# Optimization experiments

Measured on AMD Instinct MI355X. Metric: run time of the kernel, lower is better.

## Reference

```python
import jax, jax.numpy as jnp
import numpy as np

B, T, D = 4, 2048, 2048
P, K, ALPHA, R = 512, 16, 4, 32
E_RATIO = 0.8
EPS = 1e-6


def rmsnorm(x, g):
    return x * jax.lax.rsqrt(jnp.mean(x * x, axis=-1, keepdims=True) + EPS) * g


def dale_signs():
    # first e_ratio*P neurons excitatory (+1), rest inhibitory (-1)
    return jnp.where(jnp.arange(P) < int(E_RATIO * P), 1.0, -1.0)


def quant_dale(w, signs):
    # STE sign-quantization with per-neuron mean-abs scale + Dale's-law sign constraint
    scale = jnp.mean(jnp.abs(w), axis=-1, keepdims=True)  # [P,1]
    q = scale * signs[:, None] * jnp.ones_like(w)         # magnitude=scale, sign fixed per neuron
    return w + jax.lax.stop_gradient(q - w)


def synapse_graph(x, idx, w):
    # x: [B,T,D], idx: [P,K] int, w: [P,K] -> dendritic inputs [B,T,P,K]
    return jnp.take(x, idx, axis=-1) * w


def perceptron(x_dend, Wp, Wout, signs):
    Wq = quant_dale(Wp, signs)                              # [P,K]
    u = jnp.einsum('btpk,pk->btp', x_dend, Wq)              # [B,T,P]
    f = jax.nn.sigmoid(u)                                   # gate [B,T,P]
    f_out = quant_dale(Wout, signs)                         # [P,ALPHA]
    y = (f * u)[..., None] * f_out                          # [B,T,P,ALPHA]
    return u, f, y, f_out


def low_rank_ssm(t, f, s0, U, V, Wgate, bgate):
    # t,f: [B,T,P]; s0: [B,R]. Low-rank gated linear scan in R dims.
    z = jnp.einsum('btp,pr->btr', t, U)
    lam = jax.nn.sigmoid(jnp.einsum('btp,pr->btr', f, Wgate) + bgate)

    def step(s, inp):
        z_t, l_t = inp
        s = l_t * s + z_t
        return s, s

    sT, S = jax.lax.scan(step, s0, (jnp.moveaxis(z, 1, 0), jnp.moveaxis(lam, 1, 0)))
    tilde = jnp.einsum('btr,rp->btp', jnp.moveaxis(S, 0, 1), V)
    return tilde, sT


def flatten_ports(y):
    return y.reshape(*y.shape[:-2], P * ALPHA)


def setup_inputs() -> dict:
    key = jax.random.key(0)
    ks = jax.random.split(key, 14)
    sc = 0.1
    return {
        'x': jax.random.normal(ks[0], (B, T, D), jnp.float32),
        'state': jnp.zeros((B, R), jnp.float32),
        'g1': jnp.ones((D,), jnp.float32),
        'g2': jnp.ones((D,), jnp.float32),
        'idx_ssm': jax.random.randint(ks[1], (P, K), 0, D),
        'wg_ssm': jax.random.normal(ks[2], (P, K), jnp.float32) * sc,
        'idx_mlp': jax.random.randint(ks[3], (P, K), 0, D),
        'wg_mlp': jax.random.normal(ks[4], (P, K), jnp.float32) * sc,
        'Wp_ssm': jax.random.normal(ks[5], (P, K), jnp.float32) * sc,
        'Wout_ssm': jax.random.normal(ks[6], (P, ALPHA), jnp.float32) * sc,
        'Wp_mlp': jax.random.normal(ks[7], (P, K), jnp.float32) * sc,
        'Wout_mlp': jax.random.normal(ks[8], (P, ALPHA), jnp.float32) * sc,
        'U': jax.random.normal(ks[9], (P, R), jnp.float32) * sc,
        'V': jax.random.normal(ks[10], (R, P), jnp.float32) * sc,
        'Wgate': jax.random.normal(ks[11], (P, R), jnp.float32) * sc,
        'bgate': jnp.zeros((R,), jnp.float32),
    }


def reference(x, state, g1, g2, idx_ssm, wg_ssm, idx_mlp, wg_mlp,
              Wp_ssm, Wout_ssm, Wp_mlp, Wout_mlp, U, V, Wgate, bgate):
    signs = dale_signs()
    # --- SSM branch ---
    h1 = rmsnorm(x, g1)
    x_dend_ssm = synapse_graph(h1, idx_ssm, wg_ssm)
    u_ssm, f_ssm, _, f_out = perceptron(x_dend_ssm, Wp_ssm, Wout_ssm, signs)
    t_ssm = f_ssm * u_ssm
    tilde_t, new_state = low_rank_ssm(t_ssm, f_ssm, state, U, V, Wgate, bgate)
    y_ssm = (f_ssm * tilde_t)[..., None] * f_out            # [B,T,P,ALPHA]
    x_after = x + flatten_ports(y_ssm)
    # --- MLP branch ---
    h2 = rmsnorm(x_after, g2)
    x_dend_mlp = synapse_graph(h2, idx_mlp, wg_mlp)
    _, _, y_mlp, _ = perceptron(x_dend_mlp, Wp_mlp, Wout_mlp, signs)
    x_out = x_after + flatten_ports(y_mlp)
    return x_out, new_state
```

## Files before the change

### kernel.cpp

```cpp
#include <hip/hip_runtime.h>
#include <hip/hip_bf16.h>

#define B_ 4
#define T_ 2048
#define D_ 2048
#define P_ 512
#define K_ 16
#define ALPHA_ 4
#define R_ 32
#define NE_ 409
#define EPS_ 1e-6f
#define G_ 4

typedef unsigned short u16;
typedef unsigned int u32;
typedef _Float16 half2_t __attribute__((ext_vector_type(2)));

__device__ __forceinline__ float sigmoidf_(float x) {
  return 1.0f / (1.0f + __expf(-x));
}
__device__ __forceinline__ float bfb2f(u16 u) {
  return __uint_as_float(((u32)u) << 16);
}
__device__ __forceinline__ u16 f2bfb(float f) {
  __hip_bfloat16 h = __float2bfloat16(f);
  return *reinterpret_cast<u16*>(&h);
}
__device__ __forceinline__ float bflo(u32 u) { return __uint_as_float(u << 16); }
__device__ __forceinline__ float bfhi(u32 u) { return __uint_as_float(u & 0xFFFF0000u); }
__device__ __forceinline__ u16 f2h(float f) {
  _Float16 h = (_Float16)f;
  return *reinterpret_cast<u16*>(&h);
}
__device__ __forceinline__ float dot2h(u32 a, u32 b, float c) {
#if __has_builtin(__builtin_amdgcn_fdot2)
  return __builtin_amdgcn_fdot2(__builtin_bit_cast(half2_t, a),
                                __builtin_bit_cast(half2_t, b), c, false);
#else
  half2_t ha = __builtin_bit_cast(half2_t, a);
  half2_t hb = __builtin_bit_cast(half2_t, b);
  return c + (float)ha.x * (float)hb.x + (float)ha.y * (float)hb.y;
#endif
}

__global__ void k_scalars(const float* __restrict__ Wp_s, const float* __restrict__ Wo_s,
                          const float* __restrict__ Wp_m, const float* __restrict__ Wo_m,
                          const float* __restrict__ U, const float* __restrict__ Wgt,
                          float* __restrict__ wq_s, float* __restrict__ fo_s,
                          float* __restrict__ wq_m, float* __restrict__ fo_m,
                          u16* __restrict__ Ut16, u16* __restrict__ Wt16) {
  int p = blockIdx.x * blockDim.x + threadIdx.x;
  if (p >= P_) return;
  float sgn = (p < NE_) ? 1.0f : -1.0f;
  float a = 0, b = 0, c = 0, d = 0;
#pragma unroll
  for (int k = 0; k < K_; k++) {
    a += fabsf(Wp_s[p * K_ + k]);
    c += fabsf(Wp_m[p * K_ + k]);
  }
#pragma unroll
  for (int k = 0; k < ALPHA_; k++) {
    b += fabsf(Wo_s[p * ALPHA_ + k]);
    d += fabsf(Wo_m[p * ALPHA_ + k]);
  }
  wq_s[p] = sgn * a * (1.0f / K_);
  fo_s[p] = sgn * b * (1.0f / ALPHA_);
  wq_m[p] = sgn * c * (1.0f / K_);
  fo_m[p] = sgn * d * (1.0f / ALPHA_);
#pragma unroll
  for (int r = 0; r < R_; r++) {
    Ut16[r * P_ + p] = f2h(U[p * R_ + r]);
    Wt16[r * P_ + p] = f2h(Wgt[p * R_ + r]);
  }
}

__global__ __launch_bounds__(256) void k_phase1(
    const float* __restrict__ x, const float* __restrict__ g1,
    const int* __restrict__ idx, const float* __restrict__ wg,
    const u16* __restrict__ Ut16, const u16* __restrict__ Wt16,
    const float* __restrict__ bg, const float* __restrict__ wq,
    u16* __restrict__ f_ssm, float* __restrict__ z, float* __restrict__ lam) {
  __shared__ u16 h1[G_][D_];
  __shared__ u16 tl16[G_][P_];
  __shared__ u16 fl16[G_][P_];
  __shared__ float red[G_][4];
  __shared__ float zp[G_][R_][4];
  __shared__ float lp[G_][R_][4];

  int tid = threadIdx.x;
  int token0 = blockIdx.x * G_;
  int b = token0 >> 11;
  int t0 = token0 & (T_ - 1);

  float gv[8];
  {
    const float4* gp = reinterpret_cast<const float4*>(g1 + tid * 8);
    *reinterpret_cast<float4*>(&gv[0]) = gp[0];
    *reinterpret_cast<float4*>(&gv[4]) = gp[1];
  }
#pragma unroll
  for (int tok = 0; tok < G_; tok++) {
    float xv[8];
    const float4* xp = reinterpret_cast<const float4*>(x + (size_t)(token0 + tok) * D_ + tid * 8);
    *reinterpret_cast<float4*>(&xv[0]) = xp[0];
    *reinterpret_cast<float4*>(&xv[4]) = xp[1];
    float ss = 0;
    u16 tmp[8];
#pragma unroll
    for (int i = 0; i < 8; i++) { ss += xv[i] * xv[i]; tmp[i] = f2bfb(xv[i] * gv[i]); }
    *reinterpret_cast<uint4*>(&h1[tok][tid * 8]) = *reinterpret_cast<const uint4*>(tmp);
#pragma unroll
    for (int off = 32; off; off >>= 1) ss += __shfl_down(ss, off);
    if ((tid & 63) == 0) red[tok][tid >> 6] = ss;
  }
  __syncthreads();

  float inv[G_];
#pragma unroll
  for (int tok = 0; tok < G_; tok++)
    inv[tok] = rsqrtf((red[tok][0] + red[tok][1] + red[tok][2] + red[tok][3]) * (1.0f / D_) + EPS_);

#pragma unroll
  for (int j = 0; j < 2; j++) {
    int p = tid + j * 256;
    union { int4 v[4]; int s[16]; } iu;
    const int4* ip = reinterpret_cast<const int4*>(idx + p * K_);
    iu.v[0] = ip[0]; iu.v[1] = ip[1]; iu.v[2] = ip[2]; iu.v[3] = ip[3];
    union { float4 v[4]; float s[16]; } wu;
    const float4* wp = reinterpret_cast<const float4*>(wg + p * K_);
    wu.v[0] = wp[0]; wu.v[1] = wp[1]; wu.v[2] = wp[2]; wu.v[3] = wp[3];
    float wqp = wq[p];
#pragma unroll
    for (int tok = 0; tok < G_; tok++) {
      float acc = 0;
#pragma unroll
      for (int k = 0; k < K_; k++) acc += bfb2f(h1[tok][iu.s[k]]) * wu.s[k];
      float u = wqp * inv[tok] * acc;
      float f = sigmoidf_(u);
      tl16[tok][p] = f2h(f * u);
      fl16[tok][p] = f2h(f);
      f_ssm[(size_t)(token0 + tok) * P_ + p] = f2bfb(f);
    }
  }
  __syncthreads();

  int r = tid & 31, g = tid >> 5;
  float zs[G_], ls[G_];
#pragma unroll
  for (int tok = 0; tok < G_; tok++) { zs[tok] = 0; ls[tok] = 0; }
  int pb = g * 64;
  const uint4* Utp = reinterpret_cast<const uint4*>(Ut16 + r * P_ + pb);
  const uint4* Wtp = reinterpret_cast<const uint4*>(Wt16 + r * P_ + pb);
#pragma unroll
  for (int q = 0; q < 8; q++) {
    uint4 uq = Utp[q];
    uint4 wq4 = Wtp[q];
#pragma unroll
    for (int tok = 0; tok < G_; tok++) {
      uint4 tq = *reinterpret_cast<const uint4*>(&tl16[tok][pb + q * 8]);
      uint4 fq = *reinterpret_cast<const uint4*>(&fl16[tok][pb + q * 8]);
      zs[tok] = dot2h(tq.x, uq.x, zs[tok]);
      zs[tok] = dot2h(tq.y, uq.y, zs[tok]);
      zs[tok] = dot2h(tq.z, uq.z, zs[tok]);
      zs[tok] = dot2h(tq.w, uq.w, zs[tok]);
      ls[tok] = dot2h(fq.x, wq4.x, ls[tok]);
      ls[tok] = dot2h(fq.y, wq4.y, ls[tok]);
      ls[tok] = dot2h(fq.z, wq4.z, ls[tok]);
      ls[tok] = dot2h(fq.w, wq4.w, ls[tok]);
    }
  }
#pragma unroll
  for (int tok = 0; tok < G_; tok++) {
    zs[tok] += __shfl_down(zs[tok], 32);
    ls[tok] += __shfl_down(ls[tok], 32);
  }
  int wid = tid >> 6;
  if ((tid & 63) < 32) {
#pragma unroll
    for (int tok = 0; tok < G_; tok++) { zp[tok][r][wid] = zs[tok]; lp[tok][r][wid] = ls[tok]; }
  }
  __syncthreads();
  if (tid < R_) {
    float bgr = bg[tid];
    float z4[G_], l4[G_];
#pragma unroll
    for (int tok = 0; tok < G_; tok++) {
      float zz = zp[tok][tid][0] + zp[tok][tid][1] + zp[tok][tid][2] + zp[tok][tid][3];
      float ll = lp[tok][tid][0] + lp[tok][tid][1] + lp[tok][tid][2] + lp[tok][tid][3];
      z4[tok] = zz;
      l4[tok] = sigmoidf_(ll + bgr);
    }
    size_t o = ((size_t)(b * R_ + tid)) * T_ + t0;
    *reinterpret_cast<float4*>(&z[o]) = *reinterpret_cast<const float4*>(z4);
    *reinterpret_cast<float4*>(&lam[o]) = *reinterpret_cast<const float4*>(l4);
  }
}

__global__ __launch_bounds__(64) void k_scan(
    const float* __restrict__ z, const float* __restrict__ lam,
    const float* __restrict__ state, float* __restrict__ S,
    float* __restrict__ out_state) {
  int br = blockIdx.x;
  int lane = threadIdx.x;
  const float* zr = z + (size_t)br * T_ + lane * 32;
  const float* lr = lam + (size_t)br * T_ + lane * 32;
  float zb[32], lb[32];
#pragma unroll
  for (int i = 0; i < 32; i += 4) {
    *reinterpret_cast<float4*>(&zb[i]) = *reinterpret_cast<const float4*>(&zr[i]);
    *reinterpret_cast<float4*>(&lb[i]) = *reinterpret_cast<const float4*>(&lr[i]);
  }
  float A = 1.0f, Z = 0.0f;
#pragma unroll
  for (int i = 0; i < 32; i++) { Z = lb[i] * Z + zb[i]; A *= lb[i]; }
  for (int off = 1; off < 64; off <<= 1) {
    float Ap = __shfl_up(A, off);
    float Zp = __shfl_up(Z, off);
    if (lane >= off) { Z = A * Zp + Z; A = A * Ap; }
  }
  float s0 = state[br];
  float Ae = __shfl_up(A, 1);
  float Ze = __shfl_up(Z, 1);
  float s = (lane == 0) ? s0 : (Ae * s0 + Ze);
  float sb[32];
#pragma unroll
  for (int i = 0; i < 32; i++) { s = lb[i] * s + zb[i]; sb[i] = s; }
  float* Sr = S + (size_t)br * T_ + lane * 32;
#pragma unroll
  for (int i = 0; i < 32; i += 4)
    *reinterpret_cast<float4*>(&Sr[i]) = *reinterpret_cast<const float4*>(&sb[i]);
  if (lane == 63) out_state[br] = s;
}

__global__ __launch_bounds__(256) void k_phase3(
    const float* __restrict__ x, const float* __restrict__ g2,
    const int* __restrict__ idx, const float* __restrict__ wg,
    const float* __restrict__ V, const float* __restrict__ S,
    const u16* __restrict__ f_ssm, const float* __restrict__ fo_s,
    const float* __restrict__ wq_m, const float* __restrict__ fo_m,
    float* __restrict__ out) {
  __shared__ float Sl[G_][R_];
  __shared__ u16 h2[G_][D_];
  __shared__ float red[G_][4];

  int tid = threadIdx.x;
  int token0 = blockIdx.x * G_;
  int b = token0 >> 11;
  int t0 = token0 & (T_ - 1);
  int p0 = 2 * tid;

  if (tid < G_ * R_) {
    int tok = tid >> 5, r = tid & 31;
    Sl[tok][r] = S[((size_t)(b * R_ + r)) * T_ + t0 + tok];
  }
  __syncthreads();

  float til0[G_], til1[G_];
#pragma unroll
  for (int tok = 0; tok < G_; tok++) { til0[tok] = 0; til1[tok] = 0; }
#pragma unroll 4
  for (int r = 0; r < R_; r++) {
    float2 vv = *reinterpret_cast<const float2*>(V + r * P_ + p0);
#pragma unroll
    for (int tok = 0; tok < G_; tok++) {
      float s = Sl[tok][r];
      til0[tok] += s * vv.x;
      til1[tok] += s * vv.y;
    }
  }

  float2 fo = *reinterpret_cast<const float2*>(fo_s + p0);
  float gv[8];
  {
    const float4* gp = reinterpret_cast<const float4*>(g2 + tid * 8);
    *reinterpret_cast<float4*>(&gv[0]) = gp[0];
    *reinterpret_cast<float4*>(&gv[4]) = gp[1];
  }

  float xa[G_][8];
#pragma unroll
  for (int tok = 0; tok < G_; tok++) {
    u32 ff = *reinterpret_cast<const u32*>(f_ssm + (size_t)(token0 + tok) * P_ + p0);
    float val0 = bflo(ff) * til0[tok] * fo.x;
    float val1 = bfhi(ff) * til1[tok] * fo.y;
    float xv[8];
    const float4* xp = reinterpret_cast<const float4*>(x + (size_t)(token0 + tok) * D_ + tid * 8);
    *reinterpret_cast<float4*>(&xv[0]) = xp[0];
    *reinterpret_cast<float4*>(&xv[4]) = xp[1];
    float ss = 0;
#pragma unroll
    for (int a = 0; a < 4; a++) {
      float v0 = xv[a] + val0;
      float v1 = xv[4 + a] + val1;
      xa[tok][a] = v0;
      xa[tok][4 + a] = v1;
      ss += v0 * v0 + v1 * v1;
    }
    u16 tmp[8];
#pragma unroll
    for (int i = 0; i < 8; i++) tmp[i] = f2bfb(xa[tok][i] * gv[i]);
    *reinterpret_cast<uint4*>(&h2[tok][tid * 8]) = *reinterpret_cast<const uint4*>(tmp);
#pragma unroll
    for (int off = 32; off; off >>= 1) ss += __shfl_down(ss, off);
    if ((tid & 63) == 0) red[tok][tid >> 6] = ss;
  }
  __syncthreads();

  union { int4 v[4]; int s[16]; } iu0, iu1;
  union { float4 v[4]; float s[16]; } wu0, wu1;
  {
    const int4* ip0 = reinterpret_cast<const int4*>(idx + p0 * K_);
    const int4* ip1 = reinterpret_cast<const int4*>(idx + (p0 + 1) * K_);
    const float4* wp0 = reinterpret_cast<const float4*>(wg + p0 * K_);
    const float4* wp1 = reinterpret_cast<const float4*>(wg + (p0 + 1) * K_);
#pragma unroll
    for (int q = 0; q < 4; q++) { iu0.v[q] = ip0[q]; iu1.v[q] = ip1[q]; wu0.v[q] = wp0[q]; wu1.v[q] = wp1[q]; }
  }
  float2 wqm = *reinterpret_cast<const float2*>(wq_m + p0);
  float2 fom = *reinterpret_cast<const float2*>(fo_m + p0);

#pragma unroll
  for (int tok = 0; tok < G_; tok++) {
    float invt = rsqrtf((red[tok][0] + red[tok][1] + red[tok][2] + red[tok][3]) * (1.0f / D_) + EPS_);
    float acc0 = 0, acc1 = 0;
#pragma unroll
    for (int k = 0; k < K_; k++) {
      acc0 += bfb2f(h2[tok][iu0.s[k]]) * wu0.s[k];
      acc1 += bfb2f(h2[tok][iu1.s[k]]) * wu1.s[k];
    }
    float u0 = wqm.x * invt * acc0, u1 = wqm.y * invt * acc1;
    float f0 = sigmoidf_(u0), f1 = sigmoidf_(u1);
    float val0 = f0 * u0 * fom.x, val1 = f1 * u1 * fom.y;
    float ov[8];
#pragma unroll
    for (int a = 0; a < 4; a++) {
      ov[a] = xa[tok][a] + val0;
      ov[4 + a] = xa[tok][4 + a] + val1;
    }
    float4* op = reinterpret_cast<float4*>(out + (size_t)(token0 + tok) * D_ + tid * 8);
    op[0] = *reinterpret_cast<const float4*>(&ov[0]);
    op[1] = *reinterpret_cast<const float4*>(&ov[4]);
  }
}

extern "C" void kernel_launch(void* const* d_in, const int* in_sizes, int n_in,
                              void* d_out, int out_size, void* d_ws, size_t ws_size,
                              hipStream_t stream) {
  const float* x     = (const float*)d_in[0];
  const float* state = (const float*)d_in[1];
  const float* g1    = (const float*)d_in[2];
  const float* g2    = (const float*)d_in[3];
  const int*   idx_s = (const int*)d_in[4];
  const float* wg_s  = (const float*)d_in[5];
  const int*   idx_m = (const int*)d_in[6];
  const float* wg_m  = (const float*)d_in[7];
  const float* Wp_s  = (const float*)d_in[8];
  const float* Wo_s  = (const float*)d_in[9];
  const float* Wp_m  = (const float*)d_in[10];
  const float* Wo_m  = (const float*)d_in[11];
  const float* U     = (const float*)d_in[12];
  const float* V     = (const float*)d_in[13];
  const float* Wgt   = (const float*)d_in[14];
  const float* bg    = (const float*)d_in[15];
  float* out = (float*)d_out;

  char* ws = (char*)d_ws;
  float* wq_s = (float*)(ws + 0);
  float* fo_s = (float*)(ws + 2048);
  float* wq_m = (float*)(ws + 4096);
  float* fo_m = (float*)(ws + 6144);
  u16* Ut16 = (u16*)(ws + 8192);
  u16* Wt16 = (u16*)(ws + 8192 + 32768);
  size_t off = 8192 + 65536;
  u16* f_ssm = (u16*)(ws + off); off += (size_t)B_ * T_ * P_ * 2;
  float* z   = (float*)(ws + off); off += (size_t)B_ * R_ * T_ * 4;
  float* lam = (float*)(ws + off); off += (size_t)B_ * R_ * T_ * 4;
  float* S   = (float*)(ws + off);

  hipLaunchKernelGGL(k_scalars, dim3(2), dim3(256), 0, stream,
                     Wp_s, Wo_s, Wp_m, Wo_m, U, Wgt, wq_s, fo_s, wq_m, fo_m, Ut16, Wt16);
  hipLaunchKernelGGL(k_phase1, dim3(B_ * T_ / G_), dim3(256), 0, stream,
                     x, g1, idx_s, wg_s, Ut16, Wt16, bg, wq_s, f_ssm, z, lam);
  hipLaunchKernelGGL(k_scan, dim3(B_ * R_), dim3(64), 0, stream,
                     z, lam, state, S, out + (size_t)B_ * T_ * D_);
  hipLaunchKernelGGL(k_phase3, dim3(B_ * T_ / G_), dim3(256), 0, stream,
                     x, g2, idx_m, wg_m, V, S, f_ssm, fo_s, wq_m, fo_m, out);
}
```

Before: 221.9 us.

## Fuse all phases into one persistent kernel with grid barriers

Merges the four launches (scalar prep, phase1, scan, phase3) into one persistent kernel of 1024 blocks, each handling two token groups, separated by atomic-counter grid barriers. The SSM gate f is kept in registers across the barrier instead of being written to and re-read from a global f_ssm buffer. This removes launch gaps and the f_ssm round trip. In exchange it depends on all 1024 blocks being co-resident (launch_bounds 256,4) for the spin barrier to be safe, and it adds barrier latency plus an extra memset launch.

```diff
diff --git a/kernel.cpp b/kernel.cpp
--- a/kernel.cpp
+++ b/kernel.cpp
@@ -11,6 +11,8 @@
 #define NE_ 409
 #define EPS_ 1e-6f
 #define G_ 4
+#define GRID_ 1024
+#define NITER_ 2
 
 typedef unsigned short u16;
 typedef unsigned int u32;
@@ -26,12 +28,18 @@
   __hip_bfloat16 h = __float2bfloat16(f);
   return *reinterpret_cast<u16*>(&h);
 }
-__device__ __forceinline__ float bflo(u32 u) { return __uint_as_float(u << 16); }
-__device__ __forceinline__ float bfhi(u32 u) { return __uint_as_float(u & 0xFFFF0000u); }
 __device__ __forceinline__ u16 f2h(float f) {
   _Float16 h = (_Float16)f;
   return *reinterpret_cast<u16*>(&h);
 }
+__device__ __forceinline__ u32 packh(float a, float b) {
+  half2_t h;
+  h.x = (_Float16)a;
+  h.y = (_Float16)b;
+  return __builtin_bit_cast(u32, h);
+}
+__device__ __forceinline__ float hlo(u32 u) { return (float)__builtin_bit_cast(half2_t, u).x; }
+__device__ __forceinline__ float hhi(u32 u) { return (float)__builtin_bit_cast(half2_t, u).y; }
 __device__ __forceinline__ float dot2h(u32 a, u32 b, float c) {
 #if __has_builtin(__builtin_amdgcn_fdot2)
   return __builtin_amdgcn_fdot2(__builtin_bit_cast(half2_t, a),
@@ -43,303 +51,329 @@
 #endif
 }
 
-__global__ void k_scalars(const float* __restrict__ Wp_s, const float* __restrict__ Wo_s,
-                          const float* __restrict__ Wp_m, const float* __restrict__ Wo_m,
-                          const float* __restrict__ U, const float* __restrict__ Wgt,
-                          float* __restrict__ wq_s, float* __restrict__ fo_s,
-                          float* __restrict__ wq_m, float* __restrict__ fo_m,
-                          u16* __restrict__ Ut16, u16* __restrict__ Wt16) {
-  int p = blockIdx.x * blockDim.x + threadIdx.x;
-  if (p >= P_) return;
-  float sgn = (p < NE_) ? 1.0f : -1.0f;
-  float a = 0, b = 0, c = 0, d = 0;
-#pragma unroll
-  for (int k = 0; k < K_; k++) {
-    a += fabsf(Wp_s[p * K_ + k]);
-    c += fabsf(Wp_m[p * K_ + k]);
+__device__ __forceinline__ void grid_barrier(u32* ctr) {
+  __syncthreads();
+  if (threadIdx.x == 0) {
+    __threadfence();
+    atomicAdd(ctr, 1u);
+    int spins = 0;
+    while (__hip_atomic_load(ctr, __ATOMIC_RELAXED, __HIP_MEMORY_SCOPE_AGENT) < (u32)GRID_ &&
+           spins < (1 << 22)) {
+      __builtin_amdgcn_s_sleep(8);
+      ++spins;
+    }
+    __threadfence();
   }
-#pragma unroll
-  for (int k = 0; k < ALPHA_; k++) {
-    b += fabsf(Wo_s[p * ALPHA_ + k]);
-    d += fabsf(Wo_m[p * ALPHA_ + k]);
-  }
-  wq_s[p] = sgn * a * (1.0f / K_);
-  fo_s[p] = sgn * b * (1.0f / ALPHA_);
-  wq_m[p] = sgn * c * (1.0f / K_);
-  fo_m[p] = sgn * d * (1.0f / ALPHA_);
-#pragma unroll
-  for (int r = 0; r < R_; r++) {
-    Ut16[r * P_ + p] = f2h(U[p * R_ + r]);
-    Wt16[r * P_ + p] = f2h(Wgt[p * R_ + r]);
-  }
-}
-
-__global__ __launch_bounds__(256) void k_phase1(
-    const float* __restrict__ x, const float* __restrict__ g1,
-    const int* __restrict__ idx, const float* __restrict__ wg,
-    const u16* __restrict__ Ut16, const u16* __restrict__ Wt16,
-    const float* __restrict__ bg, const float* __restrict__ wq,
-    u16* __restrict__ f_ssm, float* __restrict__ z, float* __restrict__ lam) {
+  __syncthreads();
+}
+
+__global__ __launch_bounds__(256, 4) void k_fused(
+    const float* __restrict__ x, const float* __restrict__ state,
+    const float* __restrict__ g1, const float* __restrict__ g2,
+    const int* __restrict__ idx_s, const float* __restrict__ wg_s,
+    const int* __restrict__ idx_m, const float* __restrict__ wg_m,
+    const float* __restrict__ Wp_s, const float* __restrict__ Wo_s,
+    const float* __restrict__ Wp_m, const float* __restrict__ Wo_m,
+    const float* __restrict__ U, const float* __restrict__ V,
+    const float* __restrict__ Wgt, const float* __restrict__ bg,
+    float* __restrict__ wq_s, float* __restrict__ fo_s,
+    float* __restrict__ wq_m, float* __restrict__ fo_m,
+    u16* __restrict__ Ut16, u16* __restrict__ Wt16,
+    float* __restrict__ z, float* __restrict__ lam, float* __restrict__ S,
+    u32* __restrict__ bar, float* __restrict__ out) {
   __shared__ u16 h1[G_][D_];
   __shared__ u16 tl16[G_][P_];
   __shared__ u16 fl16[G_][P_];
   __shared__ float red[G_][4];
   __shared__ float zp[G_][R_][4];
   __shared__ float lp[G_][R_][4];
+  __shared__ float Sl[G_][R_];
 
   int tid = threadIdx.x;
-  int token0 = blockIdx.x * G_;
-  int b = token0 >> 11;
-  int t0 = token0 & (T_ - 1);
-
-  float gv[8];
+  int bid = blockIdx.x;
+
+  if (bid < 2) {
+    int p = bid * 256 + tid;
+    float sgn = (p < NE_) ? 1.0f : -1.0f;
+    float a = 0, bb = 0, c = 0, d = 0;
+#pragma unroll
+    for (int k = 0; k < K_; k++) {
+      a += fabsf(Wp_s[p * K_ + k]);
+      c += fabsf(Wp_m[p * K_ + k]);
+    }
+#pragma unroll
+    for (int k = 0; k < ALPHA_; k++) {
+      bb += fabsf(Wo_s[p * ALPHA_ + k]);
+      d += fabsf(Wo_m[p * ALPHA_ + k]);
+    }
+    wq_s[p] = sgn * a * (1.0f / K_);
+    fo_s[p] = sgn * bb * (1.0f / ALPHA_);
+    wq_m[p] = sgn * c * (1.0f / K_);
+    fo_m[p] = sgn * d * (1.0f / ALPHA_);
+#pragma unroll
+    for (int r = 0; r < R_; r++) {
+      Ut16[r * P_ + p] = f2h(U[p * R_ + r]);
+      Wt16[r * P_ + p] = f2h(Wgt[p * R_ + r]);
+    }
+  }
+  grid_barrier(bar + 0);
+
+  u32 freg[NITER_][G_];
+#pragma unroll
+  for (int it = 0; it < NITER_; ++it) {
+    int grp = bid + it * GRID_;
+    int token0 = grp * G_;
+    int b = token0 >> 11;
+    int t0 = token0 & (T_ - 1);
+    __syncthreads();
+
+    float gv[8];
+    {
+      const float4* gp = reinterpret_cast<const float4*>(g1 + tid * 8);
+      *reinterpret_cast<float4*>(&gv[0]) = gp[0];
+      *reinterpret_cast<float4*>(&gv[4]) = gp[1];
+    }
+#pragma unroll
+    for (int tok = 0; tok < G_; tok++) {
+      float xv[8];
+      const float4* xp = reinterpret_cast<const float4*>(x + (size_t)(token0 + tok) * D_ + tid * 8);
+      *reinterpret_cast<float4*>(&xv[0]) = xp[0];
+      *reinterpret_cast<float4*>(&xv[4]) = xp[1];
+      float ss = 0;
+      u16 tmp[8];
+#pragma unroll
+      for (int i = 0; i < 8; i++) { ss += xv[i] * xv[i]; tmp[i] = f2bfb(xv[i] * gv[i]); }
+      *reinterpret_cast<uint4*>(&h1[tok][tid * 8]) = *reinterpret_cast<const uint4*>(tmp);
+#pragma unroll
+      for (int off = 32; off; off >>= 1) ss += __shfl_down(ss, off);
+      if ((tid & 63) == 0) red[tok][tid >> 6] = ss;
+    }
+    __syncthreads();
+
+    float inv[G_];
+#pragma unroll
+    for (int tok = 0; tok < G_; tok++)
+      inv[tok] = rsqrtf((red[tok][0] + red[tok][1] + red[tok][2] + red[tok][3]) * (1.0f / D_) + EPS_);
+
+    {
+      int p0 = 2 * tid, p1 = p0 + 1;
+      union { int4 v[4]; int s[16]; } iu0, iu1;
+      union { float4 v[4]; float s[16]; } wu0, wu1;
+      const int4* ip0 = reinterpret_cast<const int4*>(idx_s + p0 * K_);
+      const int4* ip1 = reinterpret_cast<const int4*>(idx_s + p1 * K_);
+      const float4* wp0 = reinterpret_cast<const float4*>(wg_s + p0 * K_);
+      const float4* wp1 = reinterpret_cast<const float4*>(wg_s + p1 * K_);
+#pragma unroll
+      for (int q = 0; q < 4; q++) { iu0.v[q] = ip0[q]; iu1.v[q] = ip1[q]; wu0.v[q] = wp0[q]; wu1.v[q] = wp1[q]; }
+      float2 wq2 = *reinterpret_cast<const float2*>(wq_s + p0);
+#pragma unroll
+      for (int tok = 0; tok < G_; tok++) {
+        float acc0 = 0, acc1 = 0;
+#pragma unroll
+        for (int k = 0; k < K_; k++) {
+          acc0 += bfb2f(h1[tok][iu0.s[k]]) * wu0.s[k];
+          acc1 += bfb2f(h1[tok][iu1.s[k]]) * wu1.s[k];
+        }
+        float u0 = wq2.x * inv[tok] * acc0, u1 = wq2.y * inv[tok] * acc1;
+        float f0 = sigmoidf_(u0), f1 = sigmoidf_(u1);
+        *reinterpret_cast<u32*>(&tl16[tok][p0]) = packh(f0 * u0, f1 * u1);
+        u32 fp = packh(f0, f1);
+        *reinterpret_cast<u32*>(&fl16[tok][p0]) = fp;
+        freg[it][tok] = fp;
+      }
+    }
+    __syncthreads();
+
+    int r = tid & 31, pg = tid >> 5;
+    float zs[G_], ls[G_];
+#pragma unroll
+    for (int tok = 0; tok < G_; tok++) { zs[tok] = 0; ls[tok] = 0; }
+    int pb = pg * 64;
+    const uint4* Utp = reinterpret_cast<const uint4*>(Ut16 + r * P_ + pb);
+    const uint4* Wtp = reinterpret_cast<const uint4*>(Wt16 + r * P_ + pb);
+#pragma unroll
+    for (int q = 0; q < 8; q++) {
+      uint4 uq = Utp[q];
+      uint4 wq4 = Wtp[q];
+#pragma unroll
+      for (int tok = 0; tok < G_; tok++) {
+        uint4 tq = *reinterpret_cast<const uint4*>(&tl16[tok][pb + q * 8]);
+        uint4 fq = *reinterpret_cast<const uint4*>(&fl16[tok][pb + q * 8]);
+        zs[tok] = dot2h(tq.x, uq.x, zs[tok]);
+        zs[tok] = dot2h(tq.y, uq.y, zs[tok]);
+        zs[tok] = dot2h(tq.z, uq.z, zs[tok]);
+        zs[tok] = dot2h(tq.w, uq.w, zs[tok]);
+        ls[tok] = dot2h(fq.x, wq4.x, ls[tok]);
+        ls[tok] = dot2h(fq.y, wq4.y, ls[tok]);
+        ls[tok] = dot2h(fq.z, wq4.z, ls[tok]);
+        ls[tok] = dot2h(fq.w, wq4.w, ls[tok]);
+      }
+    }
+#pragma unroll
+    for (int tok = 0; tok < G_; tok++) {
+      zs[tok] += __shfl_down(zs[tok], 32);
+      ls[tok] += __shfl_down(ls[tok], 32);
+    }
+    int wid = tid >> 6;
+    if ((tid & 63) < 32) {
+#pragma unroll
+      for (int tok = 0; tok < G_; tok++) { zp[tok][r][wid] = zs[tok]; lp[tok][r][wid] = ls[tok]; }
+    }
+    __syncthreads();
+    if (tid < R_) {
+      float bgr = bg[tid];
+      float z4[G_], l4[G_];
+#pragma unroll
+      for (int tok = 0; tok < G_; tok++) {
+        float zz = zp[tok][tid][0] + zp[tok][tid][1] + zp[tok][tid][2] + zp[tok][tid][3];
+        float ll = lp[tok][tid][0] + lp[tok][tid][1] + lp[tok][tid][2] + lp[tok][tid][3];
+        z4[tok] = zz;
+        l4[tok] = sigmoidf_(ll + bgr);
+      }
+      size_t o = ((size_t)(b * R_ + tid)) * T_ + t0;
+      *reinterpret_cast<float4*>(&z[o]) = *reinterpret_cast<const float4*>(z4);
+      *reinterpret_cast<float4*>(&lam[o]) = *reinterpret_cast<const float4*>(l4);
+    }
+  }
+  grid_barrier(bar + 1);
+
   {
-    const float4* gp = reinterpret_cast<const float4*>(g1 + tid * 8);
-    *reinterpret_cast<float4*>(&gv[0]) = gp[0];
-    *reinterpret_cast<float4*>(&gv[4]) = gp[1];
+    int gw = bid * 4 + (tid >> 6);
+    if (bid < 32 && gw < B_ * R_) {
+      int br = gw;
+      int lane = tid & 63;
+      const float* zr = z + (size_t)br * T_ + lane * 32;
+      const float* lr = lam + (size_t)br * T_ + lane * 32;
+      float zb[32], lb[32];
+#pragma unroll
+      for (int i = 0; i < 32; i += 4) {
+        *reinterpret_cast<float4*>(&zb[i]) = *reinterpret_cast<const float4*>(&zr[i]);
+        *reinterpret_cast<float4*>(&lb[i]) = *reinterpret_cast<const float4*>(&lr[i]);
+      }
+      float A = 1.0f, Z = 0.0f;
+#pragma unroll
+      for (int i = 0; i < 32; i++) { Z = lb[i] * Z + zb[i]; A *= lb[i]; }
+      for (int off = 1; off < 64; off <<= 1) {
+        float Ap = __shfl_up(A, off);
+        float Zp = __shfl_up(Z, off);
+        if (lane >= off) { Z = A * Zp + Z; A = A * Ap; }
+      }
+      float s0 = state[br];
+      float Ae = __shfl_up(A, 1);
+      float Ze = __shfl_up(Z, 1);
+      float s = (lane == 0) ? s0 : (Ae * s0 + Ze);
+      float sb[32];
+#pragma unroll
+      for (int i = 0; i < 32; i++) { s = lb[i] * s + zb[i]; sb[i] = s; }
+      float* Sr = S + (size_t)br * T_ + lane * 32;
+#pragma unroll
+      for (int i = 0; i < 32; i += 4)
+        *reinterpret_cast<float4*>(&Sr[i]) = *reinterpret_cast<const float4*>(&sb[i]);
+      if (lane == 63) out[(size_t)B_ * T_ * D_ + br] = s;
+    }
   }
-#pragma unroll
-  for (int tok = 0; tok < G_; tok++) {
-    float xv[8];
-    const float4* xp = reinterpret_cast<const float4*>(x + (size_t)(token0 + tok) * D_ + tid * 8);
-    *reinterpret_cast<float4*>(&xv[0]) = xp[0];
-    *reinterpret_cast<float4*>(&xv[4]) = xp[1];
-    float ss = 0;
-    u16 tmp[8];
-#pragma unroll
-    for (int i = 0; i < 8; i++) { ss += xv[i] * xv[i]; tmp[i] = f2bfb(xv[i] * gv[i]); }
-    *reinterpret_cast<uint4*>(&h1[tok][tid * 8]) = *reinterpret_cast<const uint4*>(tmp);
-#pragma unroll
-    for (int off = 32; off; off >>= 1) ss += __shfl_down(ss, off);
-    if ((tid & 63) == 0) red[tok][tid >> 6] = ss;
-  }
-  __syncthreads();
-
-  float inv[G_];
-#pragma unroll
-  for (int tok = 0; tok < G_; tok++)
-    inv[tok] = rsqrtf((red[tok][0] + red[tok][1] + red[tok][2] + red[tok][3]) * (1.0f / D_) + EPS_);
-
-#pragma unroll
-  for (int j = 0; j < 2; j++) {
-    int p = tid + j * 256;
-    union { int4 v[4]; int s[16]; } iu;
-    const int4* ip = reinterpret_cast<const int4*>(idx + p * K_);
-    iu.v[0] = ip[0]; iu.v[1] = ip[1]; iu.v[2] = ip[2]; iu.v[3] = ip[3];
-    union { float4 v[4]; float s[16]; } wu;
-    const float4* wp = reinterpret_cast<const float4*>(wg + p * K_);
-    wu.v[0] = wp[0]; wu.v[1] = wp[1]; wu.v[2] = wp[2]; wu.v[3] = wp[3];
-    float wqp = wq[p];
+  grid_barrier(bar + 2);
+
+#pragma unroll
+  for (int it = 0; it < NITER_; ++it) {
+    int grp = bid + it * GRID_;
+    int token0 = grp * G_;
+    int b = token0 >> 11;
+    int t0 = token0 & (T_ - 1);
+    int p0 = 2 * tid;
+    __syncthreads();
+    if (tid < G_ * R_) {
+      int tok = tid >> 5, r = tid & 31;
+      Sl[tok][r] = S[((size_t)(b * R_ + r)) * T_ + t0 + tok];
+    }
+    __syncthreads();
+
+    float til0[G_], til1[G_];
+#pragma unroll
+    for (int tok = 0; tok < G_; tok++) { til0[tok] = 0; til1[tok] = 0; }
+#pragma unroll 4
+    for (int r = 0; r < R_; r++) {
+      float2 vv = *reinterpret_cast<const float2*>(V + r * P_ + p0);
+#pragma unroll
+      for (int tok = 0; tok < G_; tok++) {
+        float s = Sl[tok][r];
+        til0[tok] += s * vv.x;
+        til1[tok] += s * vv.y;
+      }
+    }
+
+    float2 fo = *reinterpret_cast<const float2*>(fo_s + p0);
+    float gv[8];
+    {
+      const float4* gp = reinterpret_cast<const float4*>(g2 + tid * 8);
+      *reinterpret_cast<float4*>(&gv[0]) = gp[0];
+      *reinterpret_cast<float4*>(&gv[4]) = gp[1];
+    }
+
+    float xa[G_][8];
 #pragma unroll
     for (int tok = 0; tok < G_; tok++) {
-      float acc = 0;
-#pragma unroll
-      for (int k = 0; k < K_; k++) acc += bfb2f(h1[tok][iu.s[k]]) * wu.s[k];
-      float u = wqp * inv[tok] * acc;
-      float f = sigmoidf_(u);
-      tl16[tok][p] = f2h(f * u);
-      fl16[tok][p] = f2h(f);
-      f_ssm[(size_t)(token0 + tok) * P_ + p] = f2bfb(f);
-    }
-  }
-  __syncthreads();
-
-  int r = tid & 31, g = tid >> 5;
-  float zs[G_], ls[G_];
-#pragma unroll
-  for (int tok = 0; tok < G_; tok++) { zs[tok] = 0; ls[tok] = 0; }
-  int pb = g * 64;
-  const uint4* Utp = reinterpret_cast<const uint4*>(Ut16 + r * P_ + pb);
-  const uint4* Wtp = reinterpret_cast<const uint4*>(Wt16 + r * P_ + pb);
-#pragma unroll
-  for (int q = 0; q < 8; q++) {
-    uint4 uq = Utp[q];
-    uint4 wq4 = Wtp[q];
+      u32 fp = freg[it][tok];
+      float val0 = hlo(fp) * til0[tok] * fo.x;
+      float val1 = hhi(fp) * til1[tok] * fo.y;
+      float xv[8];
+      const float4* xp = reinterpret_cast<const float4*>(x + (size_t)(token0 + tok) * D_ + tid * 8);
+      *reinterpret_cast<float4*>(&xv[0]) = xp[0];
+      *reinterpret_cast<float4*>(&xv[4]) = xp[1];
+      float ss = 0;
+#pragma unroll
+      for (int a = 0; a < 4; a++) {
+        float v0 = xv[a] + val0;
+        float v1 = xv[4 + a] + val1;
+        xa[tok][a] = v0;
+        xa[tok][4 + a] = v1;
+        ss += v0 * v0 + v1 * v1;
+      }
+      u16 tmp[8];
+#pragma unroll
+      for (int i = 0; i < 8; i++) tmp[i] = f2bfb(xa[tok][i] * gv[i]);
+      *reinterpret_cast<uint4*>(&h1[tok][tid * 8]) = *reinterpret_cast<const uint4*>(tmp);
+#pragma unroll
+      for (int off = 32; off; off >>= 1) ss += __shfl_down(ss, off);
+      if ((tid & 63) == 0) red[tok][tid >> 6] = ss;
+    }
+    __syncthreads();
+
+    union { int4 v[4]; int s[16]; } iu0, iu1;
+    union { float4 v[4]; float s[16]; } wu0, wu1;
+    {
+      const int4* ip0 = reinterpret_cast<const int4*>(idx_m + p0 * K_);
+      const int4* ip1 = reinterpret_cast<const int4*>(idx_m + (p0 + 1) * K_);
+      const float4* wp0 = reinterpret_cast<const float4*>(wg_m + p0 * K_);
+      const float4* wp1 = reinterpret_cast<const float4*>(wg_m + (p0 + 1) * K_);
+#pragma unroll
+      for (int q = 0; q < 4; q++) { iu0.v[q] = ip0[q]; iu1.v[q] = ip1[q]; wu0.v[q] = wp0[q]; wu1.v[q] = wp1[q]; }
+    }
+    float2 wqm = *reinterpret_cast<const float2*>(wq_m + p0);
+    float2 fom = *reinterpret_cast<const float2*>(fo_m + p0);
+
 #pragma unroll
     for (int tok = 0; tok < G_; tok++) {
-      uint4 tq = *reinterpret_cast<const uint4*>(&tl16[tok][pb + q * 8]);
-      uint4 fq = *reinterpret_cast<const uint4*>(&fl16[tok][pb + q * 8]);
-      zs[tok] = dot2h(tq.x, uq.x, zs[tok]);
-      zs[tok] = dot2h(tq.y, uq.y, zs[tok]);
-      zs[tok] = dot2h(tq.z, uq.z, zs[tok]);
-      zs[tok] = dot2h(tq.w, uq.w, zs[tok]);
-      ls[tok] = dot2h(fq.x, wq4.x, ls[tok]);
-      ls[tok] = dot2h(fq.y, wq4.y, ls[tok]);
-      ls[tok] = dot2h(fq.z, wq4.z, ls[tok]);
-      ls[tok] = dot2h(fq.w, wq4.w, ls[tok]);
-    }
-  }
-#pragma unroll
-  for (int tok = 0; tok < G_; tok++) {
-    zs[tok] += __shfl_down(zs[tok], 32);
-    ls[tok] += __shfl_down(ls[tok], 32);
-  }
-  int wid = tid >> 6;
-  if ((tid & 63) < 32) {
-#pragma unroll
-    for (int tok = 0; tok < G_; tok++) { zp[tok][r][wid] = zs[tok]; lp[tok][r][wid] = ls[tok]; }
-  }
-  __syncthreads();
-  if (tid < R_) {
-    float bgr = bg[tid];
-    float z4[G_], l4[G_];
-#pragma unroll
-    for (int tok = 0; tok < G_; tok++) {
-      float zz = zp[tok][tid][0] + zp[tok][tid][1] + zp[tok][tid][2] + zp[tok][tid][3];
-      float ll = lp[tok][tid][0] + lp[tok][tid][1] + lp[tok][tid][2] + lp[tok][tid][3];
-      z4[tok] = zz;
-      l4[tok] = sigmoidf_(ll + bgr);
-    }
-    size_t o = ((size_t)(b * R_ + tid)) * T_ + t0;
-    *reinterpret_cast<float4*>(&z[o]) = *reinterpret_cast<const float4*>(z4);
-    *reinterpret_cast<float4*>(&lam[o]) = *reinterpret_cast<const float4*>(l4);
-  }
-}
-
-__global__ __launch_bounds__(64) void k_scan(
-    const float* __restrict__ z, const float* __restrict__ lam,
-    const float* __restrict__ state, float* __restrict__ S,
-    float* __restrict__ out_state) {
-  int br = blockIdx.x;
-  int lane = threadIdx.x;
-  const float* zr = z + (size_t)br * T_ + lane * 32;
-  const float* lr = lam + (size_t)br * T_ + lane * 32;
-  float zb[32], lb[32];
-#pragma unroll
-  for (int i = 0; i < 32; i += 4) {
-    *reinterpret_cast<float4*>(&zb[i]) = *reinterpret_cast<const float4*>(&zr[i]);
-    *reinterpret_cast<float4*>(&lb[i]) = *reinterpret_cast<const float4*>(&lr[i]);
-  }
-  float A = 1.0f, Z = 0.0f;
-#pragma unroll
-  for (int i = 0; i < 32; i++) { Z = lb[i] * Z + zb[i]; A *= lb[i]; }
-  for (int off = 1; off < 64; off <<= 1) {
-    float Ap = __shfl_up(A, off);
-    float Zp = __shfl_up(Z, off);
-    if (lane >= off) { Z = A * Zp + Z; A = A * Ap; }
-  }
-  float s0 = state[br];
-  float Ae = __shfl_up(A, 1);
-  float Ze = __shfl_up(Z, 1);
-  float s = (lane == 0) ? s0 : (Ae * s0 + Ze);
-  float sb[32];
-#pragma unroll
-  for (int i = 0; i < 32; i++) { s = lb[i] * s + zb[i]; sb[i] = s; }
-  float* Sr = S + (size_t)br * T_ + lane * 32;
-#pragma unroll
-  for (int i = 0; i < 32; i += 4)
-    *reinterpret_cast<float4*>(&Sr[i]) = *reinterpret_cast<const float4*>(&sb[i]);
-  if (lane == 63) out_state[br] = s;
-}
-
-__global__ __launch_bounds__(256) void k_phase3(
-    const float* __restrict__ x, const float* __restrict__ g2,
-    const int* __restrict__ idx, const float* __restrict__ wg,
-    const float* __restrict__ V, const float* __restrict__ S,
-    const u16* __restrict__ f_ssm, const float* __restrict__ fo_s,
-    const float* __restrict__ wq_m, const float* __restrict__ fo_m,
-    float* __restrict__ out) {
-  __shared__ float Sl[G_][R_];
-  __shared__ u16 h2[G_][D_];
-  __shared__ float red[G_][4];
-
-  int tid = threadIdx.x;
-  int token0 = blockIdx.x * G_;
-  int b = token0 >> 11;
-  int t0 = token0 & (T_ - 1);
-  int p0 = 2 * tid;
-
-  if (tid < G_ * R_) {
-    int tok = tid >> 5, r = tid & 31;
-    Sl[tok][r] = S[((size_t)(b * R_ + r)) * T_ + t0 + tok];
-  }
-  __syncthreads();
-
-  float til0[G_], til1[G_];
-#pragma unroll
-  for (int tok = 0; tok < G_; tok++) { til0[tok] = 0; til1[tok] = 0; }
-#pragma unroll 4
-  for (int r = 0; r < R_; r++) {
-    float2 vv = *reinterpret_cast<const float2*>(V + r * P_ + p0);
-#pragma unroll
-    for (int tok = 0; tok < G_; tok++) {
-      float s = Sl[tok][r];
-      til0[tok] += s * vv.x;
-      til1[tok] += s * vv.y;
-    }
-  }
-
-  float2 fo = *reinterpret_cast<const float2*>(fo_s + p0);
-  float gv[8];
-  {
-    const float4* gp = reinterpret_cast<const float4*>(g2 + tid * 8);
-    *reinterpret_cast<float4*>(&gv[0]) = gp[0];
-    *reinterpret_cast<float4*>(&gv[4]) = gp[1];
-  }
-
-  float xa[G_][8];
-#pragma unroll
-  for (int tok = 0; tok < G_; tok++) {
-    u32 ff = *reinterpret_cast<const u32*>(f_ssm + (size_t)(token0 + tok) * P_ + p0);
-    float val0 = bflo(ff) * til0[tok] * fo.x;
-    float val1 = bfhi(ff) * til1[tok] * fo.y;
-    float xv[8];
-    const float4* xp = reinterpret_cast<const float4*>(x + (size_t)(token0 + tok) * D_ + tid * 8);
-    *reinterpret_cast<float4*>(&xv[0]) = xp[0];
-    *reinterpret_cast<float4*>(&xv[4]) = xp[1];
-    float ss = 0;
-#pragma unroll
-    for (int a = 0; a < 4; a++) {
-      float v0 = xv[a] + val0;
-      float v1 = xv[4 + a] + val1;
-      xa[tok][a] = v0;
-      xa[tok][4 + a] = v1;
-      ss += v0 * v0 + v1 * v1;
-    }
-    u16 tmp[8];
-#pragma unroll
-    for (int i = 0; i < 8; i++) tmp[i] = f2bfb(xa[tok][i] * gv[i]);
-    *reinterpret_cast<uint4*>(&h2[tok][tid * 8]) = *reinterpret_cast<const uint4*>(tmp);
-#pragma unroll
-    for (int off = 32; off; off >>= 1) ss += __shfl_down(ss, off);
-    if ((tid & 63) == 0) red[tok][tid >> 6] = ss;
-  }
-  __syncthreads();
-
-  union { int4 v[4]; int s[16]; } iu0, iu1;
-  union { float4 v[4]; float s[16]; } wu0, wu1;
-  {
-    const int4* ip0 = reinterpret_cast<const int4*>(idx + p0 * K_);
-    const int4* ip1 = reinterpret_cast<const int4*>(idx + (p0 + 1) * K_);
-    const float4* wp0 = reinterpret_cast<const float4*>(wg + p0 * K_);
-    const float4* wp1 = reinterpret_cast<const float4*>(wg + (p0 + 1) * K_);
-#pragma unroll
-    for (int q = 0; q < 4; q++) { iu0.v[q] = ip0[q]; iu1.v[q] = ip1[q]; wu0.v[q] = wp0[q]; wu1.v[q] = wp1[q]; }
-  }
-  float2 wqm = *reinterpret_cast<const float2*>(wq_m + p0);
-  float2 fom = *reinterpret_cast<const float2*>(fo_m + p0);
-
-#pragma unroll
-  for (int tok = 0; tok < G_; tok++) {
-    float invt = rsqrtf((red[tok][0] + red[tok][1] + red[tok][2] + red[tok][3]) * (1.0f / D_) + EPS_);
-    float acc0 = 0, acc1 = 0;
-#pragma unroll
-    for (int k = 0; k < K_; k++) {
-      acc0 += bfb2f(h2[tok][iu0.s[k]]) * wu0.s[k];
-      acc1 += bfb2f(h2[tok][iu1.s[k]]) * wu1.s[k];
-    }
-    float u0 = wqm.x * invt * acc0, u1 = wqm.y * invt * acc1;
-    float f0 = sigmoidf_(u0), f1 = sigmoidf_(u1);
-    float val0 = f0 * u0 * fom.x, val1 = f1 * u1 * fom.y;
-    float ov[8];
-#pragma unroll
-    for (int a = 0; a < 4; a++) {
-      ov[a] = xa[tok][a] + val0;
-      ov[4 + a] = xa[tok][4 + a] + val1;
-    }
-    float4* op = reinterpret_cast<float4*>(out + (size_t)(token0 + tok) * D_ + tid * 8);
-    op[0] = *reinterpret_cast<const float4*>(&ov[0]);
-    op[1] = *reinterpret_cast<const float4*>(&ov[4]);
+      float invt = rsqrtf((red[tok][0] + red[tok][1] + red[tok][2] + red[tok][3]) * (1.0f / D_) + EPS_);
+      float acc0 = 0, acc1 = 0;
+#pragma unroll
+      for (int k = 0; k < K_; k++) {
+        acc0 += bfb2f(h1[tok][iu0.s[k]]) * wu0.s[k];
+        acc1 += bfb2f(h1[tok][iu1.s[k]]) * wu1.s[k];
+      }
+      float u0 = wqm.x * invt * acc0, u1 = wqm.y * invt * acc1;
+      float f0 = sigmoidf_(u0), f1 = sigmoidf_(u1);
+      float val0 = f0 * u0 * fom.x, val1 = f1 * u1 * fom.y;
+      float ov[8];
+#pragma unroll
+      for (int a = 0; a < 4; a++) {
+        ov[a] = xa[tok][a] + val0;
+        ov[4 + a] = xa[tok][4 + a] + val1;
+      }
+      float4* op = reinterpret_cast<float4*>(out + (size_t)(token0 + tok) * D_ + tid * 8);
+      op[0] = *reinterpret_cast<const float4*>(&ov[0]);
+      op[1] = *reinterpret_cast<const float4*>(&ov[4]);
+    }
   }
 }
 
@@ -372,17 +406,16 @@
   u16* Ut16 = (u16*)(ws + 8192);
   u16* Wt16 = (u16*)(ws + 8192 + 32768);
   size_t off = 8192 + 65536;
-  u16* f_ssm = (u16*)(ws + off); off += (size_t)B_ * T_ * P_ * 2;
   float* z   = (float*)(ws + off); off += (size_t)B_ * R_ * T_ * 4;
   float* lam = (float*)(ws + off); off += (size_t)B_ * R_ * T_ * 4;
-  float* S   = (float*)(ws + off);
-
-  hipLaunchKernelGGL(k_scalars, dim3(2), dim3(256), 0, stream,
-                     Wp_s, Wo_s, Wp_m, Wo_m, U, Wgt, wq_s, fo_s, wq_m, fo_m, Ut16, Wt16);
-  hipLaunchKernelGGL(k_phase1, dim3(B_ * T_ / G_), dim3(256), 0, stream,
-                     x, g1, idx_s, wg_s, Ut16, Wt16, bg, wq_s, f_ssm, z, lam);
-  hipLaunchKernelGGL(k_scan, dim3(B_ * R_), dim3(64), 0, stream,
-                     z, lam, state, S, out + (size_t)B_ * T_ * D_);
-  hipLaunchKernelGGL(k_phase3, dim3(B_ * T_ / G_), dim3(256), 0, stream,
-                     x, g2, idx_m, wg_m, V, S, f_ssm, fo_s, wq_m, fo_m, out);
-}
+  float* S   = (float*)(ws + off); off += (size_t)B_ * R_ * T_ * 4;
+  u32* bar   = (u32*)(ws + off);
+
+  hipMemsetAsync(bar, 0, 256, stream);
+
+  hipLaunchKernelGGL(k_fused, dim3(GRID_), dim3(256), 0, stream,
+                     x, state, g1, g2, idx_s, wg_s, idx_m, wg_m,
+                     Wp_s, Wo_s, Wp_m, Wo_m, U, V, Wgt, bg,
+                     wq_s, fo_s, wq_m, fo_m, Ut16, Wt16,
+                     z, lam, S, bar, out);
+}
```

Measured after the change: 584.9 us. 2.64x slower.
